# Optimization experiments

Measured on AMD Instinct MI355X. Metric: run time of the kernel, lower is better.

The kernel has to match this reference:

```python
import jax, jax.numpy as jnp
import numpy as np

EMBED_SIZE = 512
HEADS = 8
HEAD_DIM = EMBED_SIZE // HEADS
N, SEQ = 4, 2048


def setup_inputs() -> dict:
    key = jax.random.key(0)
    ks = jax.random.split(key, 9)
    inp = {
        "values": jax.random.normal(ks[0], (N, SEQ, EMBED_SIZE), dtype=jnp.float32),
        "keys": jax.random.normal(ks[1], (N, SEQ, EMBED_SIZE), dtype=jnp.float32),
        "query": jax.random.normal(ks[2], (N, SEQ, EMBED_SIZE), dtype=jnp.float32),
        "mask": jax.random.randint(ks[3], (N, 1, SEQ, SEQ), 0, 2, dtype=jnp.int32),
        # per-head projection weights (torch Linear convention: y = x @ W.T)
        "Wv": jax.random.normal(ks[4], (HEAD_DIM, HEAD_DIM), dtype=jnp.float32) / np.sqrt(HEAD_DIM),
        "Wk": jax.random.normal(ks[5], (HEAD_DIM, HEAD_DIM), dtype=jnp.float32) / np.sqrt(HEAD_DIM),
        "Wq": jax.random.normal(ks[6], (HEAD_DIM, HEAD_DIM), dtype=jnp.float32) / np.sqrt(HEAD_DIM),
        "Wout": jax.random.normal(ks[7], (EMBED_SIZE, EMBED_SIZE), dtype=jnp.float32) / np.sqrt(EMBED_SIZE),
        "bout": jax.random.normal(ks[8], (EMBED_SIZE,), dtype=jnp.float32) * 0.01,
    }
    return inp


def reference(values, keys, query, mask, Wv, Wk, Wq, Wout, bout):
    n, q_len = query.shape[0], query.shape[1]
    k_len = keys.shape[1]
    v_len = values.shape[1]
    # split heads: (N, L, H, D)
    v = values.reshape(n, v_len, HEADS, HEAD_DIM)
    k = keys.reshape(n, k_len, HEADS, HEAD_DIM)
    q = query.reshape(n, q_len, HEADS, HEAD_DIM)
    # per-head linear projections (no bias): x @ W.T
    v = jnp.einsum('nlhd,ed->nlhe', v, Wv)
    k = jnp.einsum('nlhd,ed->nlhe', k, Wk)
    q = jnp.einsum('nlhd,ed->nlhe', q, Wq)
    # energy: (N, H, Q, K)
    energy = jnp.einsum('nqhd,nkhd->nhqk', q, k)
    energy = jnp.where(mask == 0, jnp.asarray(-1e20, energy.dtype), energy)
    # note: original scales by sqrt(embed_size), not sqrt(head_dim)
    attention = jax.nn.softmax(energy / jnp.sqrt(jnp.asarray(EMBED_SIZE, energy.dtype)), axis=3)
    out = jnp.einsum('nhql,nlhd->nqhd', attention, v).reshape(n, q_len, HEADS * HEAD_DIM)
    out = out @ Wout.T + bout
    return out
```

## Files before the change

kernel.cpp:

```cpp
#include <hip/hip_runtime.h>
#include <cstdint>

#define NTOK 4
#define SEQL 2048
#define EMB 512
#define NH 8
#define HD 64

typedef unsigned int uint32;
typedef unsigned long long uint64;
typedef __attribute__((ext_vector_type(8))) short short8;
typedef __attribute__((ext_vector_type(4))) float f32x4;

__device__ __forceinline__ short f2bf(float f) {
    union { float f; uint32 u; } v; v.f = f;
    uint32 u = v.u;
    u += 0x7fffu + ((u >> 16) & 1u);
    return (short)(u >> 16);
}

__global__ __launch_bounds__(256) void k_pack_mask(const int* __restrict__ mask,
                                                   uint32* __restrict__ mp) {
    int idx = blockIdx.x * 256 + threadIdx.x;
    int lane = threadIdx.x & 63;
    uint64 b = __ballot(mask[idx] != 0);
    if (lane == 0)  mp[idx >> 5] = (uint32)b;
    if (lane == 32) mp[idx >> 5] = (uint32)(b >> 32);
}

template <bool TR>
__global__ __launch_bounds__(256) void k_proj(const float* __restrict__ in,
                                              const float* __restrict__ W,
                                              short* __restrict__ out) {
    __shared__ float xs[64][68];
    __shared__ float ws[64][68];
    __shared__ short os[64][72];
    const int t  = threadIdx.x;
    const int l0 = blockIdx.x * 64;
    const int n  = blockIdx.y / NH, h = blockIdx.y % NH;

    #pragma unroll
    for (int p = 0; p < 4; ++p) {
        int f = t * 4 + p * 1024;
        int r = f >> 6, c = f & 63;
        *(float4*)&ws[r][c] = *(const float4*)&W[f];
        *(float4*)&xs[r][c] = *(const float4*)&in[(size_t)(n * SEQL + l0 + r) * EMB + h * HD + c];
    }
    __syncthreads();

    const int lg = t >> 4, dg = t & 15;
    float acc[4][4] = {};
    #pragma unroll
    for (int e = 0; e < 64; e += 4) {
        float4 xv[4], wv[4];
        #pragma unroll
        for (int i = 0; i < 4; ++i) xv[i] = *(const float4*)&xs[lg + 16 * i][e];
        #pragma unroll
        for (int j = 0; j < 4; ++j) wv[j] = *(const float4*)&ws[dg + 16 * j][e];
        #pragma unroll
        for (int i = 0; i < 4; ++i)
            #pragma unroll
            for (int j = 0; j < 4; ++j)
                acc[i][j] += xv[i].x * wv[j].x + xv[i].y * wv[j].y +
                             xv[i].z * wv[j].z + xv[i].w * wv[j].w;
    }
    #pragma unroll
    for (int i = 0; i < 4; ++i)
        #pragma unroll
        for (int j = 0; j < 4; ++j) {
            if (TR) os[dg + 16 * j][lg + 16 * i] = f2bf(acc[i][j]);
            else    os[lg + 16 * i][dg + 16 * j] = f2bf(acc[i][j]);
        }
    __syncthreads();

    const int r = t >> 2, c = (t & 3) * 16;
    size_t base;
    if (TR) base = ((size_t)(n * NH + h) * HD + r) * SEQL + l0 + c;
    else    base = ((size_t)(n * NH + h) * SEQL + l0 + r) * HD + c;
    *(short8*)&out[base]     = *(const short8*)&os[r][c];
    *(short8*)&out[base + 8] = *(const short8*)&os[r][c + 8];
}

__global__ __launch_bounds__(256) void k_transpose(const float* __restrict__ W,
                                                   float* __restrict__ WT) {
    __shared__ float tile[32][33];
    int tx = threadIdx.x & 31, ty = threadIdx.x >> 5;
    int x0 = blockIdx.x * 32, y0 = blockIdx.y * 32;
    #pragma unroll
    for (int i = 0; i < 4; ++i)
        tile[ty + 8 * i][tx] = W[(size_t)(y0 + ty + 8 * i) * EMB + x0 + tx];
    __syncthreads();
    #pragma unroll
    for (int i = 0; i < 4; ++i)
        WT[(size_t)(x0 + ty + 8 * i) * EMB + y0 + tx] = tile[tx][ty + 8 * i];
}

__global__ __launch_bounds__(256, 4) void k_attn(const short* __restrict__ qp,
                                                 const short* __restrict__ kp,
                                                 const short* __restrict__ vp,
                                                 const uint64* __restrict__ mp,
                                                 float* __restrict__ attn) {
    __shared__ short qs[64][72];
    __shared__ short ks[64][72];
    __shared__ short vt[64][72];
    __shared__ short ps[4][16][72];
    __shared__ uint64 ms[64];

    const int t    = threadIdx.x;
    const int w    = t >> 6;
    const int lane = t & 63;
    const int lg16 = lane >> 4;
    const int l15  = lane & 15;
    const int q0   = blockIdx.x * 64;
    const int h    = blockIdx.y, n = blockIdx.z;

    const short* qg = qp + ((size_t)(n * NH + h) * SEQL + q0) * HD;
    const short* kg = kp + (size_t)(n * NH + h) * SEQL * HD;
    const short* vg = vp + (size_t)(n * NH + h) * HD * SEQL;

    {
        const int r = t >> 2, c = (t & 3) * 16;
        *(short8*)&qs[r][c]     = *(const short8*)&qg[r * HD + c];
        *(short8*)&qs[r][c + 8] = *(const short8*)&qg[r * HD + c + 8];
    }
    __syncthreads();

    short8 qa[2];
    #pragma unroll
    for (int kstp = 0; kstp < 2; ++kstp)
        qa[kstp] = *(const short8*)&qs[w * 16 + l15][lg16 * 8 + 32 * kstp];

    float m[4], lsum[4];
    f32x4 o[4];
    #pragma unroll
    for (int r = 0; r < 4; ++r) {
        m[r] = -INFINITY; lsum[r] = 0.f;
        o[r] = (f32x4){0.f, 0.f, 0.f, 0.f};
    }
    const float sc = 0.044194173824159216f;

    for (int kt = 0; kt < SEQL / 64; ++kt) {
        __syncthreads();
        {
            const int r = t >> 2, c = (t & 3) * 16;
            *(short8*)&ks[r][c]     = *(const short8*)&kg[(kt * 64 + r) * HD + c];
            *(short8*)&ks[r][c + 8] = *(const short8*)&kg[(kt * 64 + r) * HD + c + 8];
            *(short8*)&vt[r][c]     = *(const short8*)&vg[(size_t)r * SEQL + kt * 64 + c];
            *(short8*)&vt[r][c + 8] = *(const short8*)&vg[(size_t)r * SEQL + kt * 64 + c + 8];
            if (t < 64) ms[t] = mp[(size_t)(n * SEQL + q0 + t) * (SEQL / 64) + kt];
        }
        __syncthreads();

        f32x4 s[4];
        #pragma unroll
        for (int st = 0; st < 4; ++st) {
            s[st] = (f32x4){0.f, 0.f, 0.f, 0.f};
            #pragma unroll
            for (int kstp = 0; kstp < 2; ++kstp) {
                short8 kb = *(const short8*)&ks[st * 16 + l15][lg16 * 8 + 32 * kstp];
                s[st] = __builtin_amdgcn_mfma_f32_16x16x32_bf16(qa[kstp], kb, s[st], 0, 0, 0);
            }
        }

        uint64 mw[4];
        #pragma unroll
        for (int r = 0; r < 4; ++r)
            mw[r] = ms[w * 16 + lg16 * 4 + r];
        #pragma unroll
        for (int st = 0; st < 4; ++st)
            #pragma unroll
            for (int r = 0; r < 4; ++r)
                s[st][r] = ((mw[r] >> (st * 16 + l15)) & 1ULL) ? s[st][r] * sc : -1e20f;

        float pr[4][4];
        #pragma unroll
        for (int r = 0; r < 4; ++r) {
            float rm = fmaxf(fmaxf(s[0][r], s[1][r]), fmaxf(s[2][r], s[3][r]));
            rm = fmaxf(rm, __shfl_xor(rm, 1));
            rm = fmaxf(rm, __shfl_xor(rm, 2));
            rm = fmaxf(rm, __shfl_xor(rm, 4));
            rm = fmaxf(rm, __shfl_xor(rm, 8));
            float mn   = fmaxf(m[r], rm);
            float corr = __expf(m[r] - mn);
            float rs = 0.f;
            #pragma unroll
            for (int st = 0; st < 4; ++st) { pr[st][r] = __expf(s[st][r] - mn); rs += pr[st][r]; }
            rs += __shfl_xor(rs, 1); rs += __shfl_xor(rs, 2);
            rs += __shfl_xor(rs, 4); rs += __shfl_xor(rs, 8);
            lsum[r] = lsum[r] * corr + rs;
            m[r] = mn;
            #pragma unroll
            for (int dt = 0; dt < 4; ++dt) o[dt][r] *= corr;
        }

        #pragma unroll
        for (int st = 0; st < 4; ++st)
            #pragma unroll
            for (int r = 0; r < 4; ++r)
                ps[w][lg16 * 4 + r][st * 16 + l15] = f2bf(pr[st][r]);

        short8 pa[2];
        #pragma unroll
        for (int kstp = 0; kstp < 2; ++kstp)
            pa[kstp] = *(const short8*)&ps[w][l15][lg16 * 8 + 32 * kstp];
        #pragma unroll
        for (int dt = 0; dt < 4; ++dt) {
            #pragma unroll
            for (int kstp = 0; kstp < 2; ++kstp) {
                short8 vb = *(const short8*)&vt[dt * 16 + l15][lg16 * 8 + 32 * kstp];
                o[dt] = __builtin_amdgcn_mfma_f32_16x16x32_bf16(pa[kstp], vb, o[dt], 0, 0, 0);
            }
        }
    }

    float* ab = attn + ((size_t)(n * SEQL) + q0 + w * 16) * EMB + h * HD;
    #pragma unroll
    for (int r = 0; r < 4; ++r) {
        float inv = 1.0f / lsum[r];
        int row = lg16 * 4 + r;
        #pragma unroll
        for (int dt = 0; dt < 4; ++dt)
            ab[(size_t)row * EMB + dt * 16 + l15] = o[dt][r] * inv;
    }
}

__global__ __launch_bounds__(256) void k_outproj(const float* __restrict__ x,
                                                 const float* __restrict__ WT,
                                                 const float* __restrict__ bias,
                                                 float* __restrict__ out) {
    __shared__ float xs[8][EMB];
    const int t  = threadIdx.x;
    const int r0 = blockIdx.x * 8;
    #pragma unroll
    for (int p = 0; p < 4; ++p) {
        int f = (t + p * 256) * 4;
        int r = f >> 9, c = f & 511;
        *(float4*)&xs[r][c] = *(const float4*)&x[(size_t)(r0 + r) * EMB + c];
    }
    __syncthreads();

    float acc0[8] = {}, acc1[8] = {};
    for (int e = 0; e < EMB; e += 4) {
        float4 xv[8];
        #pragma unroll
        for (int r = 0; r < 8; ++r) xv[r] = *(const float4*)&xs[r][e];
        #pragma unroll
        for (int ee = 0; ee < 4; ++ee) {
            float w0 = WT[(size_t)(e + ee) * EMB + t];
            float w1 = WT[(size_t)(e + ee) * EMB + t + 256];
            #pragma unroll
            for (int r = 0; r < 8; ++r) {
                float xe = (ee == 0) ? xv[r].x : (ee == 1) ? xv[r].y : (ee == 2) ? xv[r].z : xv[r].w;
                acc0[r] += xe * w0;
                acc1[r] += xe * w1;
            }
        }
    }
    float b0 = bias[t], b1 = bias[t + 256];
    #pragma unroll
    for (int r = 0; r < 8; ++r) {
        out[(size_t)(r0 + r) * EMB + t]       = acc0[r] + b0;
        out[(size_t)(r0 + r) * EMB + t + 256] = acc1[r] + b1;
    }
}

extern "C" void kernel_launch(void* const* d_in, const int* in_sizes, int n_in,
                              void* d_out, int out_size, void* d_ws, size_t ws_size,
                              hipStream_t stream) {
    (void)in_sizes; (void)n_in; (void)out_size; (void)ws_size;
    const float* values = (const float*)d_in[0];
    const float* keys   = (const float*)d_in[1];
    const float* query  = (const float*)d_in[2];
    const int*   mask   = (const int*)d_in[3];
    const float* Wv     = (const float*)d_in[4];
    const float* Wk     = (const float*)d_in[5];
    const float* Wq     = (const float*)d_in[6];
    const float* Wout   = (const float*)d_in[7];
    const float* bout   = (const float*)d_in[8];
    float* out = (float*)d_out;

    const size_t NT = (size_t)NTOK * NH * SEQL * HD;
    short* qp = (short*)d_ws;
    short* kp = qp + NT;
    short* vp = kp + NT;
    float* at = (float*)(vp + NT);
    float* wt = at + NT;
    uint32* mpk = (uint32*)(wt + (size_t)EMB * EMB);

    k_pack_mask<<<(NTOK * SEQL * SEQL) / 256, 256, 0, stream>>>(mask, mpk);
    k_proj<false><<<dim3(SEQL / 64, NTOK * NH), 256, 0, stream>>>(query,  Wq, qp);
    k_proj<false><<<dim3(SEQL / 64, NTOK * NH), 256, 0, stream>>>(keys,   Wk, kp);
    k_proj<true ><<<dim3(SEQL / 64, NTOK * NH), 256, 0, stream>>>(values, Wv, vp);
    k_transpose<<<dim3(16, 16), 256, 0, stream>>>(Wout, wt);
    k_attn<<<dim3(SEQL / 64, NH, NTOK), 256, 0, stream>>>(qp, kp, vp, (const uint64*)mpk, at);
    k_outproj<<<(NTOK * SEQL) / 8, 256, 0, stream>>>(at, wt, bout, out);
}
```

Baseline: 427.1 us.

## Rewrite attention kernel with 32x32 MFMA, async LDS double buffering, and swizzle

The attention kernel now handles 128 query rows per block, 32 per wave. It uses 32x32x16 bf16 MFMAs computing S^T so each lane owns one query row, and stages K/V tiles into XOR-swizzled LDS with global_load_lds into a double buffer, prefetching the next tile while the current one is computed. Softmax uses exp2 with a folded scale, the P fragment is rebuilt in registers via cross-half shuffles instead of an LDS round trip, and blocks are remapped for cache locality. The aims are fewer LDS stores and barriers, overlap of memory loads with compute, and fewer row-reduction shuffles, at the cost of higher register pressure (occupancy hint drops from 4 to 2) and fewer blocks in the grid.

```diff
diff --git a/kernel.cpp b/kernel.cpp
--- a/kernel.cpp
+++ b/kernel.cpp
@@ -10,13 +10,19 @@
 typedef unsigned int uint32;
 typedef unsigned long long uint64;
 typedef __attribute__((ext_vector_type(8))) short short8;
-typedef __attribute__((ext_vector_type(4))) float f32x4;
-
-__device__ __forceinline__ short f2bf(float f) {
+typedef __attribute__((ext_vector_type(16))) float f32x16;
+
+union frag_u { uint32 u[4]; short8 s; };
+
+__device__ __forceinline__ unsigned short f2bf(float f) {
     union { float f; uint32 u; } v; v.f = f;
     uint32 u = v.u;
     u += 0x7fffu + ((u >> 16) & 1u);
-    return (short)(u >> 16);
+    return (unsigned short)(u >> 16);
+}
+
+__device__ __forceinline__ uint32 pkbf16(float a, float b) {
+    return ((uint32)f2bf(b) << 16) | (uint32)f2bf(a);
 }
 
 __global__ __launch_bounds__(256) void k_pack_mask(const int* __restrict__ mask,
@@ -68,8 +74,9 @@
     for (int i = 0; i < 4; ++i)
         #pragma unroll
         for (int j = 0; j < 4; ++j) {
-            if (TR) os[dg + 16 * j][lg + 16 * i] = f2bf(acc[i][j]);
-            else    os[lg + 16 * i][dg + 16 * j] = f2bf(acc[i][j]);
+            short sv = (short)f2bf(acc[i][j]);
+            if (TR) os[dg + 16 * j][lg + 16 * i] = sv;
+            else    os[lg + 16 * i][dg + 16 * j] = sv;
         }
     __syncthreads();
 
@@ -95,133 +102,165 @@
         WT[(size_t)(x0 + ty + 8 * i) * EMB + y0 + tx] = tile[tx][ty + 8 * i];
 }
 
-__global__ __launch_bounds__(256, 4) void k_attn(const short* __restrict__ qp,
+__device__ __forceinline__ void stage64x64(const short* __restrict__ gbase, int rstride,
+                                           short* ldst, int t) {
+    #pragma unroll
+    for (int p = 0; p < 2; ++p) {
+        int i = p * 256 + t;
+        int row = i >> 3, c = i & 7;
+        const short* src = gbase + (size_t)row * rstride + ((c ^ (row & 7)) << 3);
+        short* dst = ldst + ((i & ~63) << 3);
+        __builtin_amdgcn_global_load_lds((const __attribute__((address_space(1))) uint32*)src,
+                                         (__attribute__((address_space(3))) uint32*)dst,
+                                         16, 0, 0);
+    }
+}
+
+__global__ __launch_bounds__(256, 2) void k_attn(const short* __restrict__ qp,
                                                  const short* __restrict__ kp,
                                                  const short* __restrict__ vp,
                                                  const uint64* __restrict__ mp,
                                                  float* __restrict__ attn) {
-    __shared__ short qs[64][72];
-    __shared__ short ks[64][72];
-    __shared__ short vt[64][72];
-    __shared__ short ps[4][16][72];
-    __shared__ uint64 ms[64];
+    __shared__ short lds[2][2][64 * 64];
 
     const int t    = threadIdx.x;
+    const int lane = t & 63;
     const int w    = t >> 6;
-    const int lane = t & 63;
-    const int lg16 = lane >> 4;
-    const int l15  = lane & 15;
-    const int q0   = blockIdx.x * 64;
-    const int h    = blockIdx.y, n = blockIdx.z;
-
-    const short* qg = qp + ((size_t)(n * NH + h) * SEQL + q0) * HD;
+    const int hi   = lane >> 5;
+    const int l31  = lane & 31;
+
+    int d  = (blockIdx.z * NH + blockIdx.y) * (SEQL / 128) + blockIdx.x;
+    int lb = (d & 7) * 64 + (d >> 3);
+    const int qt = lb & 15;
+    const int h  = (lb >> 4) & 7;
+    const int n  = lb >> 7;
+    const int q0 = qt * 128;
+
+    const short* qg = qp + (size_t)(n * NH + h) * SEQL * HD;
     const short* kg = kp + (size_t)(n * NH + h) * SEQL * HD;
     const short* vg = vp + (size_t)(n * NH + h) * HD * SEQL;
 
-    {
-        const int r = t >> 2, c = (t & 3) * 16;
-        *(short8*)&qs[r][c]     = *(const short8*)&qg[r * HD + c];
-        *(short8*)&qs[r][c + 8] = *(const short8*)&qg[r * HD + c + 8];
-    }
-    __syncthreads();
-
-    short8 qa[2];
-    #pragma unroll
-    for (int kstp = 0; kstp < 2; ++kstp)
-        qa[kstp] = *(const short8*)&qs[w * 16 + l15][lg16 * 8 + 32 * kstp];
-
-    float m[4], lsum[4];
-    f32x4 o[4];
-    #pragma unroll
-    for (int r = 0; r < 4; ++r) {
-        m[r] = -INFINITY; lsum[r] = 0.f;
-        o[r] = (f32x4){0.f, 0.f, 0.f, 0.f};
-    }
-    const float sc = 0.044194173824159216f;
-
+    const int qrow = q0 + w * 32 + l31;
+
+    short8 qf[4];
+    #pragma unroll
+    for (int st = 0; st < 4; ++st)
+        qf[st] = *(const short8*)&qg[(size_t)qrow * HD + st * 16 + hi * 8];
+
+    f32x16 o0 = (f32x16)0.0f, o1 = (f32x16)0.0f;
+    float mrun = -3.0e38f, lsum = 0.0f;
+    const float c2 = 0.06376303932318478f;
+
+    stage64x64(kg, HD, &lds[0][0][0], t);
+    stage64x64(vg, SEQL, &lds[0][1][0], t);
+    __syncthreads();
+
+    int cur = 0;
+    #pragma unroll 1
     for (int kt = 0; kt < SEQL / 64; ++kt) {
+        uint64 mw = mp[((size_t)(n * SEQL) + qrow) * 32 + kt];
+        if (kt < SEQL / 64 - 1) {
+            stage64x64(kg + (kt + 1) * 64 * HD, HD, &lds[cur ^ 1][0][0], t);
+            stage64x64(vg + (kt + 1) * 64, SEQL, &lds[cur ^ 1][1][0], t);
+        }
+        const short* ks = &lds[cur][0][0];
+        const short* vs = &lds[cur][1][0];
+
+        f32x16 s0 = (f32x16)0.0f, s1 = (f32x16)0.0f;
+        #pragma unroll
+        for (int st = 0; st < 4; ++st) {
+            int ch = ((2 * st + hi) ^ (l31 & 7)) << 3;
+            short8 kf0 = *(const short8*)&ks[l31 * 64 + ch];
+            s0 = __builtin_amdgcn_mfma_f32_32x32x16_bf16(kf0, qf[st], s0, 0, 0, 0);
+            short8 kf1 = *(const short8*)&ks[(32 + l31) * 64 + ch];
+            s1 = __builtin_amdgcn_mfma_f32_32x32x16_bf16(kf1, qf[st], s1, 0, 0, 0);
+        }
+
+        uint32 m0w = (uint32)(mw >> (4 * hi));
+        uint32 m1w = (uint32)(mw >> (32 + 4 * hi));
+        #pragma unroll
+        for (int g = 0; g < 4; ++g)
+            #pragma unroll
+            for (int b = 0; b < 4; ++b) {
+                int r = g * 4 + b;
+                s0[r] = ((m0w >> (8 * g + b)) & 1u) ? s0[r] : -1e20f;
+                s1[r] = ((m1w >> (8 * g + b)) & 1u) ? s1[r] : -1e20f;
+            }
+
+        float mx[8];
+        #pragma unroll
+        for (int i = 0; i < 8; ++i)
+            mx[i] = fmaxf(fmaxf(s0[i], s0[i + 8]), fmaxf(s1[i], s1[i + 8]));
+        float rm = fmaxf(fmaxf(fmaxf(mx[0], mx[1]), fmaxf(mx[2], mx[3])),
+                         fmaxf(fmaxf(mx[4], mx[5]), fmaxf(mx[6], mx[7])));
+        rm = fmaxf(rm, __shfl_xor(rm, 32));
+        float mn   = fmaxf(mrun, rm);
+        float mnc  = mn * c2;
+        float corr = __builtin_amdgcn_exp2f(mrun * c2 - mnc);
+
+        #pragma unroll
+        for (int r = 0; r < 16; ++r) {
+            s0[r] = __builtin_amdgcn_exp2f(__builtin_fmaf(s0[r], c2, -mnc));
+            s1[r] = __builtin_amdgcn_exp2f(__builtin_fmaf(s1[r], c2, -mnc));
+        }
+
+        float sm[8];
+        #pragma unroll
+        for (int i = 0; i < 8; ++i)
+            sm[i] = (s0[i] + s0[i + 8]) + (s1[i] + s1[i + 8]);
+        float rs = ((sm[0] + sm[1]) + (sm[2] + sm[3])) + ((sm[4] + sm[5]) + (sm[6] + sm[7]));
+        rs += __shfl_xor(rs, 32);
+        lsum = lsum * corr + rs;
+        mrun = mn;
+        #pragma unroll
+        for (int r = 0; r < 16; ++r) { o0[r] *= corr; o1[r] *= corr; }
+
+        frag_u pf[4];
+        #pragma unroll
+        for (int half = 0; half < 2; ++half) {
+            const f32x16& sv = half ? s1 : s0;
+            #pragma unroll
+            for (int grp = 0; grp < 2; ++grp) {
+                uint32 x0 = pkbf16(sv[8 * grp + 0], sv[8 * grp + 1]);
+                uint32 x1 = pkbf16(sv[8 * grp + 2], sv[8 * grp + 3]);
+                uint32 y0 = pkbf16(sv[8 * grp + 4], sv[8 * grp + 5]);
+                uint32 y1 = pkbf16(sv[8 * grp + 6], sv[8 * grp + 7]);
+                uint32 sx0 = __shfl_xor(x0, 32), sx1 = __shfl_xor(x1, 32);
+                uint32 sy0 = __shfl_xor(y0, 32), sy1 = __shfl_xor(y1, 32);
+                frag_u& f = pf[half * 2 + grp];
+                f.u[0] = hi ? sy0 : x0;
+                f.u[1] = hi ? sy1 : x1;
+                f.u[2] = hi ? y0  : sx0;
+                f.u[3] = hi ? y1  : sx1;
+            }
+        }
+
+        #pragma unroll
+        for (int k4 = 0; k4 < 4; ++k4) {
+            int ch = ((2 * k4 + hi) ^ (l31 & 7)) << 3;
+            short8 vf0 = *(const short8*)&vs[l31 * 64 + ch];
+            o0 = __builtin_amdgcn_mfma_f32_32x32x16_bf16(vf0, pf[k4].s, o0, 0, 0, 0);
+            short8 vf1 = *(const short8*)&vs[(32 + l31) * 64 + ch];
+            o1 = __builtin_amdgcn_mfma_f32_32x32x16_bf16(vf1, pf[k4].s, o1, 0, 0, 0);
+        }
+
         __syncthreads();
-        {
-            const int r = t >> 2, c = (t & 3) * 16;
-            *(short8*)&ks[r][c]     = *(const short8*)&kg[(kt * 64 + r) * HD + c];
-            *(short8*)&ks[r][c + 8] = *(const short8*)&kg[(kt * 64 + r) * HD + c + 8];
-            *(short8*)&vt[r][c]     = *(const short8*)&vg[(size_t)r * SEQL + kt * 64 + c];
-            *(short8*)&vt[r][c + 8] = *(const short8*)&vg[(size_t)r * SEQL + kt * 64 + c + 8];
-            if (t < 64) ms[t] = mp[(size_t)(n * SEQL + q0 + t) * (SEQL / 64) + kt];
-        }
-        __syncthreads();
-
-        f32x4 s[4];
-        #pragma unroll
-        for (int st = 0; st < 4; ++st) {
-            s[st] = (f32x4){0.f, 0.f, 0.f, 0.f};
-            #pragma unroll
-            for (int kstp = 0; kstp < 2; ++kstp) {
-                short8 kb = *(const short8*)&ks[st * 16 + l15][lg16 * 8 + 32 * kstp];
-                s[st] = __builtin_amdgcn_mfma_f32_16x16x32_bf16(qa[kstp], kb, s[st], 0, 0, 0);
-            }
-        }
-
-        uint64 mw[4];
-        #pragma unroll
-        for (int r = 0; r < 4; ++r)
-            mw[r] = ms[w * 16 + lg16 * 4 + r];
-        #pragma unroll
-        for (int st = 0; st < 4; ++st)
-            #pragma unroll
-            for (int r = 0; r < 4; ++r)
-                s[st][r] = ((mw[r] >> (st * 16 + l15)) & 1ULL) ? s[st][r] * sc : -1e20f;
-
-        float pr[4][4];
-        #pragma unroll
-        for (int r = 0; r < 4; ++r) {
-            float rm = fmaxf(fmaxf(s[0][r], s[1][r]), fmaxf(s[2][r], s[3][r]));
-            rm = fmaxf(rm, __shfl_xor(rm, 1));
-            rm = fmaxf(rm, __shfl_xor(rm, 2));
-            rm = fmaxf(rm, __shfl_xor(rm, 4));
-            rm = fmaxf(rm, __shfl_xor(rm, 8));
-            float mn   = fmaxf(m[r], rm);
-            float corr = __expf(m[r] - mn);
-            float rs = 0.f;
-            #pragma unroll
-            for (int st = 0; st < 4; ++st) { pr[st][r] = __expf(s[st][r] - mn); rs += pr[st][r]; }
-            rs += __shfl_xor(rs, 1); rs += __shfl_xor(rs, 2);
-            rs += __shfl_xor(rs, 4); rs += __shfl_xor(rs, 8);
-            lsum[r] = lsum[r] * corr + rs;
-            m[r] = mn;
-            #pragma unroll
-            for (int dt = 0; dt < 4; ++dt) o[dt][r] *= corr;
-        }
-
-        #pragma unroll
-        for (int st = 0; st < 4; ++st)
-            #pragma unroll
-            for (int r = 0; r < 4; ++r)
-                ps[w][lg16 * 4 + r][st * 16 + l15] = f2bf(pr[st][r]);
-
-        short8 pa[2];
-        #pragma unroll
-        for (int kstp = 0; kstp < 2; ++kstp)
-            pa[kstp] = *(const short8*)&ps[w][l15][lg16 * 8 + 32 * kstp];
-        #pragma unroll
-        for (int dt = 0; dt < 4; ++dt) {
-            #pragma unroll
-            for (int kstp = 0; kstp < 2; ++kstp) {
-                short8 vb = *(const short8*)&vt[dt * 16 + l15][lg16 * 8 + 32 * kstp];
-                o[dt] = __builtin_amdgcn_mfma_f32_16x16x32_bf16(pa[kstp], vb, o[dt], 0, 0, 0);
-            }
-        }
-    }
-
-    float* ab = attn + ((size_t)(n * SEQL) + q0 + w * 16) * EMB + h * HD;
-    #pragma unroll
-    for (int r = 0; r < 4; ++r) {
-        float inv = 1.0f / lsum[r];
-        int row = lg16 * 4 + r;
-        #pragma unroll
-        for (int dt = 0; dt < 4; ++dt)
-            ab[(size_t)row * EMB + dt * 16 + l15] = o[dt][r] * inv;
-    }
+        cur ^= 1;
+    }
+
+    float inv = 1.0f / lsum;
+    float* ab = attn + ((size_t)(n * SEQL) + qrow) * EMB + h * HD;
+    #pragma unroll
+    for (int dt = 0; dt < 2; ++dt)
+        #pragma unroll
+        for (int g = 0; g < 4; ++g) {
+            float4 v;
+            v.x = (dt ? o1[4 * g + 0] : o0[4 * g + 0]) * inv;
+            v.y = (dt ? o1[4 * g + 1] : o0[4 * g + 1]) * inv;
+            v.z = (dt ? o1[4 * g + 2] : o0[4 * g + 2]) * inv;
+            v.w = (dt ? o1[4 * g + 3] : o0[4 * g + 3]) * inv;
+            *(float4*)&ab[dt * 32 + 8 * g + 4 * hi] = v;
+        }
 }
 
 __global__ __launch_bounds__(256) void k_outproj(const float* __restrict__ x,
@@ -292,6 +331,6 @@
     k_proj<false><<<dim3(SEQL / 64, NTOK * NH), 256, 0, stream>>>(keys,   Wk, kp);
     k_proj<true ><<<dim3(SEQL / 64, NTOK * NH), 256, 0, stream>>>(values, Wv, vp);
     k_transpose<<<dim3(16, 16), 256, 0, stream>>>(Wout, wt);
-    k_attn<<<dim3(SEQL / 64, NH, NTOK), 256, 0, stream>>>(qp, kp, vp, (const uint64*)mpk, at);
+    k_attn<<<dim3(SEQL / 128, NH, NTOK), 256, 0, stream>>>(qp, kp, vp, (const uint64*)mpk, at);
     k_outproj<<<(NTOK * SEQL) / 8, 256, 0, stream>>>(at, wt, bout, out);
 }
```

New measurement: 379.6 us. 1.13x faster.
